# Kernel optimization log

Hardware: AMD Instinct MI355X
Metric: run time of the kernel (lower is better)

## Reference

```python
import jax, jax.numpy as jnp
import numpy as np

IN, OUT, SPLIT = 4096, 4096, 1024

def setup_inputs() -> dict:
    key = jax.random.key(0)
    ks = jax.random.split(key, 15)
    def n(k, shape, scale=0.02):
        return jax.random.normal(k, shape, dtype=jnp.float32) * scale
    inp = {
        'x':   jax.random.normal(ks[0], (4, 2048, IN), dtype=jnp.float32),
        'V':   n(ks[1], (SPLIT, IN)),
        'U':   n(ks[2], (OUT, SPLIT)),
        'v2':  n(ks[3], (1, IN), 1.0),
        'v1':  n(ks[4], (1, SPLIT), 1.0),
        'u2':  n(ks[5], (1, SPLIT), 1.0),
        'u1':  n(ks[6], (1, OUT), 1.0),
        'V_R': n(ks[7], (SPLIT, IN)),
        'U_R': n(ks[8], (OUT, SPLIT)),
        'v2_R': n(ks[9], (1, IN), 1.0),
        'v1_R': n(ks[10], (1, SPLIT), 1.0),
        'u2_R': n(ks[11], (1, SPLIT), 1.0),
        'u1_R': n(ks[12], (1, OUT), 1.0),
        'bias': n(ks[13], (OUT,), 1.0),
    }
    return inp

def _branch(xf, V, U, v2, v1, u2, u1):
    # quantize (binarize) the two low-rank factors
    Vq = jnp.sign(V)  # [split, in]
    Uq = jnp.sign(U)  # [out, split]
    # y = ((x * v2) @ Vq.T) * (v1*u2) @ Uq.T * u1
    h = (xf * v2) @ Vq.T          # [N, split]
    h = h * (v1 * u2)             # [N, split]
    return (h @ Uq.T) * u1        # [N, out]

def reference(x, V, U, v2, v1, u2, u1, V_R, U_R, v2_R, v1_R, u2_R, u1_R, bias):
    *lead, hidden = x.shape
    xf = x.reshape(-1, hidden)
    y = _branch(xf, V, U, v2, v1, u2, u1)
    y = y + _branch(xf, V_R, U_R, v2_R, v1_R, u2_R, u1_R)
    y = y + bias
    return y.reshape(*lead, -1)
```

## Files before the change

### kernel.cpp

```cpp
#include <hip/hip_runtime.h>
#include <hip/hip_bf16.h>
#include <stdint.h>


typedef __bf16 bf16x8 __attribute__((ext_vector_type(8)));
typedef float f32x4 __attribute__((ext_vector_type(4)));

__device__ __forceinline__ void async_copy16(const void* g, void* l) {
  __builtin_amdgcn_global_load_lds(
      (const __attribute__((address_space(1))) uint32_t*)g,
      (__attribute__((address_space(3))) uint32_t*)l,
      16, 0, 0);
}

__device__ __forceinline__ float sgn(float v) {
  return (v > 0.f) ? 1.f : ((v < 0.f) ? -1.f : 0.f);
}

__device__ __forceinline__ void store_out(float* p, float v) { *p = v; }
__device__ __forceinline__ void store_out(__hip_bfloat16* p, float v) { *p = __float2bfloat16(v); }

__global__ __launch_bounds__(256) void convert_x(const float* __restrict__ x,
                                                 __hip_bfloat16* __restrict__ xb,
                                                 int n) {
  int i = (blockIdx.x * 256 + threadIdx.x) * 8;
  if (i >= n) return;
  const float4* p0 = (const float4*)(x + i);
  float4 a = p0[0], b = p0[1];
  __hip_bfloat16 o[8] = {
      __float2bfloat16(a.x), __float2bfloat16(a.y), __float2bfloat16(a.z), __float2bfloat16(a.w),
      __float2bfloat16(b.x), __float2bfloat16(b.y), __float2bfloat16(b.z), __float2bfloat16(b.w)};
  *(uint4*)(xb + i) = *(const uint4*)o;
}

__global__ __launch_bounds__(256) void prep_w1(
    const float* __restrict__ V, const float* __restrict__ v2,
    const float* __restrict__ v1, const float* __restrict__ u2,
    const float* __restrict__ V_R, const float* __restrict__ v2_R,
    const float* __restrict__ v1_R, const float* __restrict__ u2_R,
    __hip_bfloat16* __restrict__ W) {
  int g = blockIdx.x * 256 + threadIdx.x;
  int k = (g & 511) * 8;
  int s = g >> 9;
  const float *Vp, *v2p;
  float rs;
  if (s < 1024) {
    Vp = V + s * 4096 + k; v2p = v2 + k; rs = v1[s] * u2[s];
  } else {
    int ss = s - 1024;
    Vp = V_R + ss * 4096 + k; v2p = v2_R + k; rs = v1_R[ss] * u2_R[ss];
  }
  __hip_bfloat16 o[8];
#pragma unroll
  for (int e = 0; e < 8; ++e)
    o[e] = __float2bfloat16(sgn(Vp[e]) * v2p[e] * rs);
  *(uint4*)(W + s * 4096 + k) = *(const uint4*)o;
}

__global__ __launch_bounds__(256) void prep_w2(
    const float* __restrict__ U, const float* __restrict__ u1,
    const float* __restrict__ U_R, const float* __restrict__ u1_R,
    __hip_bfloat16* __restrict__ W) {
  int g = blockIdx.x * 256 + threadIdx.x;
  int s = (g & 255) * 8;
  int j = g >> 8;
  const float* Up;
  float sc;
  if (s < 1024) { Up = U + j * 1024 + s;            sc = u1[j]; }
  else          { Up = U_R + j * 1024 + (s - 1024); sc = u1_R[j]; }
  __hip_bfloat16 o[8];
#pragma unroll
  for (int e = 0; e < 8; ++e)
    o[e] = __float2bfloat16(sgn(Up[e]) * sc);
  *(uint4*)(W + j * 2048 + s) = *(const uint4*)o;
}

template <typename OutT>
__global__ __launch_bounds__(512, 2) void gemm_bt(
    const __hip_bfloat16* __restrict__ A,
    const __hip_bfloat16* __restrict__ Bt,
    OutT* __restrict__ C,
    const float* __restrict__ bias,
    int K, int N) {
  __shared__ char smem[65536];
  const int t = threadIdx.x;
  const int lane = t & 63;
  const int w = t >> 6;
  const int wm = (w >> 2) << 7;
  const int wn = (w & 3) << 6;

  const int gx = gridDim.x;
  const int gy = gridDim.y;
  const int nwg = gx * gy;
  int lin = blockIdx.y * gx + blockIdx.x;
  {
    const int xcd = lin & 7, idx = lin >> 3, q = nwg >> 3;
    lin = xcd * q + idx;
  }
  const int grpsz = gy << 1;
  const int cg = lin / grpsz;
  const int rem = lin - cg * grpsz;
  const int bm = (rem >> 1) << 8;
  const int bn = ((cg << 1) + (rem & 1)) << 8;

  const int quad = lane >> 4;
  const int l16 = lane & 15;

  f32x4 acc[8][4] = {};

  const int srow = t & 255, sch = t >> 8;
  const __hip_bfloat16* gA0 = A + (bm + srow) * K + sch * 8;
  const __hip_bfloat16* gB0 = Bt + (bn + srow) * K + sch * 8;
  const int oA0 = t * 16,          oA1 = (t + 512) * 16;
  const int oB0 = 16384 + t * 16,  oB1 = 16384 + (t + 512) * 16;

  auto stage = [&](int k0, int bufOff) {
    char* base = smem + bufOff;
    async_copy16(gA0 + k0, base + oA0);
    async_copy16(gA0 + k0 + 16, base + oA1);
    async_copy16(gB0 + k0, base + oB0);
    async_copy16(gB0 + k0 + 16, base + oB1);
  };
  auto compute = [&](int bufOff) {
    const char* base = smem + bufOff;
    bf16x8 a[8], b[4];
#pragma unroll
    for (int i = 0; i < 8; ++i)
      a[i] = *(const bf16x8*)(base + ((quad << 8) + wm + (i << 4) + l16) * 16);
#pragma unroll
    for (int j = 0; j < 4; ++j)
      b[j] = *(const bf16x8*)(base + 16384 + ((quad << 8) + wn + (j << 4) + l16) * 16);
#pragma unroll
    for (int i = 0; i < 8; ++i)
#pragma unroll
      for (int j = 0; j < 4; ++j)
        acc[i][j] = __builtin_amdgcn_mfma_f32_16x16x32_bf16(a[i], b[j], acc[i][j], 0, 0, 0);
  };

  const int NT = K >> 5;
  stage(0, 0);
  int cur = 0;
  for (int tt = 0; tt < NT; ++tt) {
    if (tt > 0) {
      __builtin_amdgcn_s_barrier();
      asm volatile("" ::: "memory");
    }
    if (tt + 1 < NT) {
      stage((tt + 1) << 5, cur ^ 32768);
      asm volatile("s_waitcnt vmcnt(4)" ::: "memory");
    } else {
      asm volatile("s_waitcnt vmcnt(0)" ::: "memory");
    }
    __builtin_amdgcn_s_barrier();
    asm volatile("" ::: "memory");
    compute(cur);
    cur ^= 32768;
  }

#pragma unroll
  for (int j = 0; j < 4; ++j) {
    int col = bn + wn + (j << 4) + l16;
    float bv = bias ? bias[col] : 0.0f;
#pragma unroll
    for (int i = 0; i < 8; ++i) {
      int row0 = bm + wm + (i << 4) + (quad << 2);
#pragma unroll
      for (int r = 0; r < 4; ++r)
        store_out(&C[(row0 + r) * N + col], acc[i][j][r] + bv);
    }
  }
}

extern "C" void kernel_launch(void* const* d_in, const int* in_sizes, int n_in,
                              void* d_out, int out_size, void* d_ws, size_t ws_size,
                              hipStream_t stream) {
  const float* x    = (const float*)d_in[0];
  const float* V    = (const float*)d_in[1];
  const float* U    = (const float*)d_in[2];
  const float* v2   = (const float*)d_in[3];
  const float* v1   = (const float*)d_in[4];
  const float* u2   = (const float*)d_in[5];
  const float* u1   = (const float*)d_in[6];
  const float* V_R  = (const float*)d_in[7];
  const float* U_R  = (const float*)d_in[8];
  const float* v2_R = (const float*)d_in[9];
  const float* v1_R = (const float*)d_in[10];
  const float* u2_R = (const float*)d_in[11];
  const float* u1_R = (const float*)d_in[12];
  const float* bias = (const float*)d_in[13];

  __hip_bfloat16* Xb  = (__hip_bfloat16*)d_ws;
  __hip_bfloat16* Wb1 = Xb + 8192 * 4096;
  __hip_bfloat16* Wb2 = Wb1 + 2048 * 4096;
  __hip_bfloat16* H   = Wb2 + 4096 * 2048;
  float* Y = (float*)d_out;

  const int nx = 8192 * 4096;
  convert_x<<<nx / (256 * 8), 256, 0, stream>>>(x, Xb, nx);
  prep_w1<<<4096, 256, 0, stream>>>(V, v2, v1, u2, V_R, v2_R, v1_R, u2_R, Wb1);
  prep_w2<<<4096, 256, 0, stream>>>(U, u1, U_R, u1_R, Wb2);

  gemm_bt<__hip_bfloat16><<<dim3(2048 / 256, 8192 / 256), 512, 0, stream>>>(
      Xb, Wb1, H, nullptr, 4096, 2048);
  gemm_bt<float><<<dim3(4096 / 256, 8192 / 256), 512, 0, stream>>>(
      H, Wb2, Y, bias, 2048, 4096);
}
```

Baseline: 689.2 us.

## Restructure GEMM mainloop into fine-grained phased pipeline with 64-wide K tiles

Rewrites the bf16 GEMM main loop to use 64-element K tiles in a 128KB double-buffered LDS. Each K step is split into four phases that interleave partial A/B async loads with MFMA work, separated by barriers, and MFMA sections are wrapped in s_setprio. The aim is to hide global-to-LDS latency and cut per-iteration barrier overhead relative to the earlier 32-wide K loop. LDS use doubles, so the launch bound of 2 workgroups per CU may no longer be reachable, which reduces occupancy. The extra barriers per phase also add synchronization cost.

```diff
diff --git a/kernel.cpp b/kernel.cpp
--- a/kernel.cpp
+++ b/kernel.cpp
@@ -75,6 +75,37 @@
   *(uint4*)(W + j * 2048 + s) = *(const uint4*)o;
 }
 
+#define PHASE(Q, BUF, LOADB, STAGE)                                            \
+  {                                                                            \
+    if (LOADB) {                                                               \
+      _Pragma("unroll") for (int j = 0; j < 4; ++j) {                          \
+        bfr[j][0] = ldb(BUF, j, 0);                                            \
+        bfr[j][1] = ldb(BUF, j, 1);                                            \
+      }                                                                        \
+    }                                                                          \
+    bf16x8 a00 = lda(BUF, 2 * (Q), 0), a01 = lda(BUF, 2 * (Q), 1);             \
+    bf16x8 a10 = lda(BUF, 2 * (Q) + 1, 0), a11 = lda(BUF, 2 * (Q) + 1, 1);     \
+    STAGE;                                                                     \
+    asm volatile("" ::: "memory");                                             \
+    __builtin_amdgcn_s_barrier();                                              \
+    asm volatile("" ::: "memory");                                             \
+    __builtin_amdgcn_s_setprio(1);                                             \
+    _Pragma("unroll") for (int j = 0; j < 4; ++j) {                            \
+      acc[2 * (Q)][j] = __builtin_amdgcn_mfma_f32_16x16x32_bf16(               \
+          a00, bfr[j][0], acc[2 * (Q)][j], 0, 0, 0);                           \
+      acc[2 * (Q)][j] = __builtin_amdgcn_mfma_f32_16x16x32_bf16(               \
+          a01, bfr[j][1], acc[2 * (Q)][j], 0, 0, 0);                           \
+      acc[2 * (Q) + 1][j] = __builtin_amdgcn_mfma_f32_16x16x32_bf16(           \
+          a10, bfr[j][0], acc[2 * (Q) + 1][j], 0, 0, 0);                       \
+      acc[2 * (Q) + 1][j] = __builtin_amdgcn_mfma_f32_16x16x32_bf16(           \
+          a11, bfr[j][1], acc[2 * (Q) + 1][j], 0, 0, 0);                       \
+    }                                                                          \
+    __builtin_amdgcn_s_setprio(0);                                             \
+    asm volatile("" ::: "memory");                                             \
+    __builtin_amdgcn_s_barrier();                                              \
+    asm volatile("" ::: "memory");                                             \
+  }
+
 template <typename OutT>
 __global__ __launch_bounds__(512, 2) void gemm_bt(
     const __hip_bfloat16* __restrict__ A,
@@ -82,7 +113,7 @@
     OutT* __restrict__ C,
     const float* __restrict__ bias,
     int K, int N) {
-  __shared__ char smem[65536];
+  __shared__ char smem[131072];
   const int t = threadIdx.x;
   const int lane = t & 63;
   const int w = t >> 6;
@@ -107,54 +138,67 @@
   const int l16 = lane & 15;
 
   f32x4 acc[8][4] = {};
-
-  const int srow = t & 255, sch = t >> 8;
-  const __hip_bfloat16* gA0 = A + (bm + srow) * K + sch * 8;
-  const __hip_bfloat16* gB0 = Bt + (bn + srow) * K + sch * 8;
-  const int oA0 = t * 16,          oA1 = (t + 512) * 16;
-  const int oB0 = 16384 + t * 16,  oB1 = 16384 + (t + 512) * 16;
-
-  auto stage = [&](int k0, int bufOff) {
-    char* base = smem + bufOff;
-    async_copy16(gA0 + k0, base + oA0);
-    async_copy16(gA0 + k0 + 16, base + oA1);
-    async_copy16(gB0 + k0, base + oB0);
-    async_copy16(gB0 + k0 + 16, base + oB1);
-  };
-  auto compute = [&](int bufOff) {
-    const char* base = smem + bufOff;
-    bf16x8 a[8], b[4];
-#pragma unroll
-    for (int i = 0; i < 8; ++i)
-      a[i] = *(const bf16x8*)(base + ((quad << 8) + wm + (i << 4) + l16) * 16);
-#pragma unroll
-    for (int j = 0; j < 4; ++j)
-      b[j] = *(const bf16x8*)(base + 16384 + ((quad << 8) + wn + (j << 4) + l16) * 16);
-#pragma unroll
-    for (int i = 0; i < 8; ++i)
-#pragma unroll
-      for (int j = 0; j < 4; ++j)
-        acc[i][j] = __builtin_amdgcn_mfma_f32_16x16x32_bf16(a[i], b[j], acc[i][j], 0, 0, 0);
-  };
-
-  const int NT = K >> 5;
-  stage(0, 0);
-  int cur = 0;
-  for (int tt = 0; tt < NT; ++tt) {
-    if (tt > 0) {
-      __builtin_amdgcn_s_barrier();
-      asm volatile("" ::: "memory");
-    }
-    if (tt + 1 < NT) {
-      stage((tt + 1) << 5, cur ^ 32768);
-      asm volatile("s_waitcnt vmcnt(4)" ::: "memory");
-    } else {
-      asm volatile("s_waitcnt vmcnt(0)" ::: "memory");
-    }
-    __builtin_amdgcn_s_barrier();
-    asm volatile("" ::: "memory");
-    compute(cur);
-    cur ^= 32768;
+  bf16x8 bfr[4][2];
+
+  const __hip_bfloat16* gAb = A + bm * K;
+  const __hip_bfloat16* gBb = Bt + bn * K;
+
+  auto stageA = [&](int k0, int half, int bufOff) {
+#pragma unroll
+    for (int r = 0; r < 2; ++r)
+      async_copy16(gAb + (half * 128 + r * 64 + lane) * K + k0 + w * 8,
+                   smem + bufOff + w * 4096 + half * 2048 + r * 1024 + lane * 16);
+  };
+  auto stageB = [&](int k0, int half, int bufOff) {
+#pragma unroll
+    for (int r = 0; r < 2; ++r)
+      async_copy16(gBb + (half * 128 + r * 64 + lane) * K + k0 + w * 8,
+                   smem + bufOff + 32768 + w * 4096 + half * 2048 + r * 1024 + lane * 16);
+  };
+  auto lda = [&](int bufOff, int i, int s) -> bf16x8 {
+    return *(const bf16x8*)(smem + bufOff + ((s << 2) + quad) * 4096 +
+                            ((wm + (i << 4) + l16) << 4));
+  };
+  auto ldb = [&](int bufOff, int j, int s) -> bf16x8 {
+    return *(const bf16x8*)(smem + bufOff + 32768 + ((s << 2) + quad) * 4096 +
+                            ((wn + (j << 4) + l16) << 4));
+  };
+
+  const int NI = K >> 7;
+
+  stageA(0, 0, 0);
+  stageA(0, 1, 0);
+  stageB(0, 0, 0);
+  stageB(0, 1, 0);
+  stageB(64, 0, 65536);
+  stageB(64, 1, 65536);
+  asm volatile("s_waitcnt vmcnt(4)" ::: "memory");
+  __builtin_amdgcn_s_barrier();
+  asm volatile("" ::: "memory");
+
+  for (int i = 0; i < NI; ++i) {
+    const int kT = i << 7;
+    const bool full = (i + 1 < NI);
+    PHASE(0, 0, true,  { stageA(kT + 64, 0, 65536); })
+    PHASE(1, 0, false, { stageA(kT + 64, 1, 65536); })
+    PHASE(2, 0, false, { if (full) stageB(kT + 128, 0, 0); })
+    PHASE(3, 0, false, {
+      if (full) {
+        stageB(kT + 128, 1, 0);
+        asm volatile("s_waitcnt vmcnt(4)" ::: "memory");
+      } else {
+        asm volatile("s_waitcnt vmcnt(0)" ::: "memory");
+      }
+    })
+    PHASE(0, 65536, true,  { if (full) stageA(kT + 128, 0, 0); })
+    PHASE(1, 65536, false, { if (full) stageA(kT + 128, 1, 0); })
+    PHASE(2, 65536, false, { if (full) stageB(kT + 192, 0, 65536); })
+    PHASE(3, 65536, false, {
+      if (full) {
+        stageB(kT + 192, 1, 65536);
+        asm volatile("s_waitcnt vmcnt(4)" ::: "memory");
+      }
+    })
   }
 
 #pragma unroll
```

Result: faster. 582.2 us (-15.5%).
